# Performance work log

Measured on AMD Instinct MI355X. Metric: run time of the kernel, lower is better.

## Reference

```python
import jax, jax.numpy as jnp
import numpy as np

EPS = 1e-05


def project_to_poincare_ball(v, eps=EPS):
    # clip norm to < 1 - eps
    norm = jnp.linalg.norm(v, axis=-1, keepdims=True)
    scale = jnp.minimum((1.0 - eps) / (norm + 1e-10), 1.0)
    return v * scale


def setup_inputs() -> dict:
    key = jax.random.key(0)
    k1, k2 = jax.random.split(key)
    B, S, D, V = 2, 2048, 512, 32000
    # scale by 0.02 so typical norms (~0.45) lie inside the unit ball
    hidden_states = jax.random.normal(k1, (B, S, D), dtype=jnp.float32) * 0.02
    weight = jax.random.normal(k2, (V, D), dtype=jnp.float32) * 0.02
    return {"hidden_states": hidden_states, "weight": weight}


def reference(hidden_states, weight):
    eps = EPS
    B, S, D = hidden_states.shape
    x = hidden_states.reshape(-1, D)                 # (N, D)
    x = project_to_poincare_ball(x, eps)
    y = project_to_poincare_ball(weight, eps)        # (V, D)

    x_norm_sq = jnp.sum(x * x, axis=-1, keepdims=True)   # (N, 1)
    y_norm_sq = jnp.sum(y * y, axis=-1)                  # (V,)

    # torch.cdist(p=2, use_mm_for_euclid_dist): ||x-y|| via mm expansion,
    # clamped at 0 before sqrt. NOTE: original code names this diff_norm_sq
    # but it is the (unsquared) distance -- reproduced faithfully.
    sq = x_norm_sq + y_norm_sq[None, :] - 2.0 * (x @ y.T)   # (N, V)
    dist = jnp.sqrt(jnp.maximum(sq, 0.0))

    denom = (1.0 - x_norm_sq) * (1.0 - y_norm_sq)[None, :]  # (N, V)
    argument = 1.0 + 2.0 * dist / (denom + eps)
    argument = jnp.maximum(argument, 1.0 + eps)
    distances = jnp.arccosh(argument)                       # (N, V)

    logits = -distances
    return logits.reshape(B, S, -1)
```

## Files before the change

kernel.cpp:

```cpp
#include <hip/hip_runtime.h>
#include <hip/hip_bf16.h>

#define D_DIM 512
#define EPS 1e-5f
#define BM 128
#define BN 128
#define BK 32
#define KT 16

typedef __attribute__((ext_vector_type(8))) short bf16x8;
typedef __attribute__((ext_vector_type(4))) float f32x4;

__device__ __forceinline__ unsigned short f2bf(float f) {
  unsigned int u = __float_as_uint(f);
  u += 0x7FFFu + ((u >> 16) & 1u);
  return (unsigned short)(u >> 16);
}

__global__ __launch_bounds__(256) void prep_rows2(
    const float* __restrict__ x, const float* __restrict__ w,
    unsigned short* __restrict__ Xbf, unsigned short* __restrict__ Ybf,
    float* __restrict__ xnsq, float* __restrict__ ynsq, int N, int total)
{
  int row  = blockIdx.x * 4 + (threadIdx.x >> 6);
  int lane = threadIdx.x & 63;
  if (row >= total) return;

  const float* src; unsigned short* dst; float* nsq; int r;
  if (row < N) { src = x; dst = Xbf; nsq = xnsq; r = row; }
  else         { src = w; dst = Ybf; nsq = ynsq; r = row - N; }

  const float4* s = (const float4*)(src + (size_t)r * D_DIM);
  float4 v0 = s[lane];
  float4 v1 = s[lane + 64];
  float ss = v0.x*v0.x + v0.y*v0.y + v0.z*v0.z + v0.w*v0.w
           + v1.x*v1.x + v1.y*v1.y + v1.z*v1.z + v1.w*v1.w;
  #pragma unroll
  for (int off = 32; off; off >>= 1) ss += __shfl_xor(ss, off);

  float norm  = sqrtf(ss);
  float scale = fminf((1.0f - EPS) / (norm + 1e-10f), 1.0f);
  if (lane == 0) nsq[r] = ss * scale * scale;

  ushort4 o0, o1;
  o0.x = f2bf(v0.x * scale); o0.y = f2bf(v0.y * scale);
  o0.z = f2bf(v0.z * scale); o0.w = f2bf(v0.w * scale);
  o1.x = f2bf(v1.x * scale); o1.y = f2bf(v1.y * scale);
  o1.z = f2bf(v1.z * scale); o1.w = f2bf(v1.w * scale);

  ushort4* dp = (ushort4*)(dst + (size_t)r * D_DIM);
  dp[lane]      = o0;
  dp[lane + 64] = o1;
}

__global__ __launch_bounds__(256, 3) void hyp_gemm(
    const unsigned short* __restrict__ Xbf, const unsigned short* __restrict__ Ybf,
    const float* __restrict__ xnsq, const float* __restrict__ ynsq,
    float* __restrict__ out, int N, int V)
{
  __shared__ __attribute__((aligned(16))) unsigned short sAB[3][2 * BM * BK];

  int ntV = V / BN;
  int bid = blockIdx.x;

  int local = bid >> 3;
  int bn = local >> 2;
  int bm = (bid & 7) * 4 + (local & 3);

  int tid  = threadIdx.x;
  int wid  = tid >> 6;
  int lane = tid & 63;
  int wm = wid >> 1, wn = wid & 1;

  size_t a_row0 = (size_t)bm * BM;
  size_t b_row0 = (size_t)bn * BN;

  auto STAGE = [&](int slot, int kt) {
    int k0 = kt * BK;
    #pragma unroll
    for (int i = 0; i < 2; ++i) {
      int c = i * 256 + tid;
      const unsigned short* gA = Xbf + (a_row0 + (size_t)(c >> 2)) * D_DIM + k0 + (c & 3) * 8;
      const unsigned short* gB = Ybf + (b_row0 + (size_t)(c >> 2)) * D_DIM + k0 + (c & 3) * 8;
      char* base = (char*)&sAB[slot][0];
      char* lA = base + (size_t)(i * 256 + wid * 64) * 16;
      char* lB = base + 8192 + (size_t)(i * 256 + wid * 64) * 16;
      __builtin_amdgcn_global_load_lds(
          (const __attribute__((address_space(1))) void*)gA,
          (__attribute__((address_space(3))) void*)lA, 16, 0, 0);
      __builtin_amdgcn_global_load_lds(
          (const __attribute__((address_space(1))) void*)gB,
          (__attribute__((address_space(3))) void*)lB, 16, 0, 0);
    }
  };

  int jr = lane & 15;
  int h  = lane >> 4;
  float xnv[4], dxv[4];
  #pragma unroll
  for (int m = 0; m < 4; ++m) {
    float xn = xnsq[bm * BM + wm * 64 + m * 16 + jr];
    xnv[m] = xn; dxv[m] = 1.0f - xn;
  }
  f32x4 ynv[4], dyv[4];
  #pragma unroll
  for (int n = 0; n < 4; ++n) {
    f32x4 y4 = *(const f32x4*)&ynsq[bn * BN + wn * 64 + n * 16 + h * 4];
    ynv[n] = y4;
    dyv[n] = 1.0f - y4;
  }

  f32x4 acc[4][4] = {};
  int r = lane & 15, ko = (lane >> 4) * 8;

  STAGE(0, 0);
  STAGE(1, 1);

  #pragma unroll
  for (int t = 0; t < KT; ++t) {
    if (t == KT - 1) {
      asm volatile("s_waitcnt vmcnt(0)" ::: "memory");
    } else {
      asm volatile("s_waitcnt vmcnt(4)" ::: "memory");
    }
    __builtin_amdgcn_sched_barrier(0);
    __builtin_amdgcn_s_barrier();
    __builtin_amdgcn_sched_barrier(0);

    const unsigned short* sA = &sAB[t % 3][0];
    const unsigned short* sB = sA + BM * BK;
    bf16x8 a[4], b[4];
    #pragma unroll
    for (int m = 0; m < 4; ++m)
      a[m] = *(const bf16x8*)&sA[(wm * 64 + m * 16 + r) * BK + ko];
    #pragma unroll
    for (int n = 0; n < 4; ++n)
      b[n] = *(const bf16x8*)&sB[(wn * 64 + n * 16 + r) * BK + ko];

    if (t + 2 < KT) STAGE((t + 2) % 3, t + 2);

    #pragma unroll
    for (int m = 0; m < 4; ++m)
      #pragma unroll
      for (int n = 0; n < 4; ++n)
        acc[m][n] = __builtin_amdgcn_mfma_f32_16x16x32_bf16(b[n], a[m], acc[m][n], 0, 0, 0);
  }

  __syncthreads();
  float* epi = (float*)&sAB[0][0] + wid * (16 * 68);

  float cmv[4];
  #pragma unroll
  for (int m = 0; m < 4; ++m) cmv[m] = 2.0f * __builtin_amdgcn_rcpf(dxv[m]);
  f32x4 rdy[4];
  #pragma unroll
  for (int n = 0; n < 4; ++n) {
    #pragma unroll
    for (int q = 0; q < 4; ++q) rdy[n][q] = __builtin_amdgcn_rcpf(dyv[n][q]);
  }

  size_t out_row0 = (size_t)bm * BM + wm * 64;
  int    out_col0 = bn * BN + wn * 64;

  #pragma unroll
  for (int m = 0; m < 4; ++m) {
    float xn = xnv[m], cm = cmv[m];
    #pragma unroll
    for (int n = 0; n < 4; ++n) {
      f32x4 f;
      #pragma unroll
      for (int q = 0; q < 4; ++q) {
        float dot  = acc[m][n][q];
        float sq   = fmaxf(xn + ynv[n][q] - 2.0f * dot, 0.0f);
        float dist = __builtin_amdgcn_sqrtf(sq);
        float arg  = fmaf(dist * cm, rdy[n][q], 1.0f);
        arg = fmaxf(arg, 1.0f + EPS);
        float t2 = __builtin_amdgcn_sqrtf(fmaf(arg, arg, -1.0f));
        f[q] = -__logf(arg + t2);
      }
      *(f32x4*)&epi[jr * 68 + n * 16 + h * 4] = f;
    }
    #pragma unroll
    for (int k = 0; k < 4; ++k) {
      int xl = k * 4 + h;
      f32x4 f = *(const f32x4*)&epi[xl * 68 + jr * 4];
      size_t rg = out_row0 + m * 16 + xl;
      int    cg = out_col0 + jr * 4;
      __builtin_nontemporal_store(f, (f32x4*)(out + rg * (size_t)V + cg));
    }
  }
}

extern "C" void kernel_launch(void* const* d_in, const int* in_sizes, int n_in,
                              void* d_out, int out_size, void* d_ws, size_t ws_size,
                              hipStream_t stream) {
  const float* x = (const float*)d_in[0];
  const float* w = (const float*)d_in[1];
  float* out = (float*)d_out;

  int N = in_sizes[0] / D_DIM;
  int V = in_sizes[1] / D_DIM;

  char* ws = (char*)d_ws;
  unsigned short* Xbf = (unsigned short*)ws;
  size_t xbf_bytes = (size_t)N * D_DIM * 2;
  unsigned short* Ybf = (unsigned short*)(ws + xbf_bytes);
  size_t ybf_bytes = (size_t)V * D_DIM * 2;
  float* xnsq = (float*)(ws + xbf_bytes + ybf_bytes);
  float* ynsq = xnsq + N;

  int total = N + V;
  prep_rows2<<<dim3((total + 3) / 4), dim3(256), 0, stream>>>(
      x, w, Xbf, Ybf, xnsq, ynsq, N, total);

  int nwg = (N / BM) * (V / BN);
  hyp_gemm<<<dim3(nwg), dim3(256), 0, stream>>>(Xbf, Ybf, xnsq, ynsq, out, N, V);
}
```

Before: 230.0 us.

## Give each wave private LDS tiles, drop block barriers, swizzle LDS slots

Each wave now stages its own 64-row A and B slices into a private double-buffered LDS region, so the per-iteration block-wide s_barrier and the pre-epilogue __syncthreads are removed. An XOR swizzle on the 16-byte k-slot is applied on the global_load_lds side and matched on the fragment reads to reduce LDS bank conflicts. The block-ID mapping drops the grouped raster for a simple row-major tile order, and occupancy is lowered to 2 blocks per CU because LDS use grows. The trade-off is that A and B tiles shared across waves are now loaded twice from global/L2, and the simpler raster may hurt L2 reuse.

Result: slower. 265.7 us (+15.5%).

```diff
diff --git a/kernel.cpp b/kernel.cpp
--- a/kernel.cpp
+++ b/kernel.cpp
@@ -53,44 +53,47 @@
   dp[lane + 64] = o1;
 }
 
-__global__ __launch_bounds__(256, 3) void hyp_gemm(
+__global__ __launch_bounds__(256, 2) void hyp_gemm(
     const unsigned short* __restrict__ Xbf, const unsigned short* __restrict__ Ybf,
     const float* __restrict__ xnsq, const float* __restrict__ ynsq,
     float* __restrict__ out, int N, int V)
 {
-  __shared__ __attribute__((aligned(16))) unsigned short sAB[3][2 * BM * BK];
-
-  int ntV = V / BN;
+  __shared__ __attribute__((aligned(16))) unsigned short lds[4][2][4096];
+
   int bid = blockIdx.x;
-
-  int local = bid >> 3;
-  int bn = local >> 2;
-  int bm = (bid & 7) * 4 + (local & 3);
+  int bm = bid & 31;
+  int bn = bid >> 5;
 
   int tid  = threadIdx.x;
   int wid  = tid >> 6;
   int lane = tid & 63;
   int wm = wid >> 1, wn = wid & 1;
 
-  size_t a_row0 = (size_t)bm * BM;
-  size_t b_row0 = (size_t)bn * BN;
-
-  auto STAGE = [&](int slot, int kt) {
+  size_t a_row0 = (size_t)bm * BM + wm * 64;
+  size_t b_row0 = (size_t)bn * BN + wn * 64;
+
+  auto STAGE = [&](int buf, int kt) {
     int k0 = kt * BK;
-    #pragma unroll
-    for (int i = 0; i < 2; ++i) {
-      int c = i * 256 + tid;
-      const unsigned short* gA = Xbf + (a_row0 + (size_t)(c >> 2)) * D_DIM + k0 + (c & 3) * 8;
-      const unsigned short* gB = Ybf + (b_row0 + (size_t)(c >> 2)) * D_DIM + k0 + (c & 3) * 8;
-      char* base = (char*)&sAB[slot][0];
-      char* lA = base + (size_t)(i * 256 + wid * 64) * 16;
-      char* lB = base + 8192 + (size_t)(i * 256 + wid * 64) * 16;
+    char* base = (char*)&lds[wid][buf][0];
+    #pragma unroll
+    for (int j = 0; j < 4; ++j) {
+      int c = j * 64 + lane;
+      int row = c >> 2;
+      int s = (c & 3) ^ ((row >> 1) & 3);
+      const unsigned short* g = Xbf + (a_row0 + row) * D_DIM + k0 + s * 8;
       __builtin_amdgcn_global_load_lds(
-          (const __attribute__((address_space(1))) void*)gA,
-          (__attribute__((address_space(3))) void*)lA, 16, 0, 0);
+          (const __attribute__((address_space(1))) void*)g,
+          (__attribute__((address_space(3))) void*)(base + j * 1024), 16, 0, 0);
+    }
+    #pragma unroll
+    for (int j = 0; j < 4; ++j) {
+      int c = j * 64 + lane;
+      int row = c >> 2;
+      int s = (c & 3) ^ ((row >> 1) & 3);
+      const unsigned short* g = Ybf + (b_row0 + row) * D_DIM + k0 + s * 8;
       __builtin_amdgcn_global_load_lds(
-          (const __attribute__((address_space(1))) void*)gB,
-          (__attribute__((address_space(3))) void*)lB, 16, 0, 0);
+          (const __attribute__((address_space(1))) void*)g,
+          (__attribute__((address_space(3))) void*)(base + 4096 + j * 1024), 16, 0, 0);
     }
   };
 
@@ -111,7 +114,8 @@
   }
 
   f32x4 acc[4][4] = {};
-  int r = lane & 15, ko = (lane >> 4) * 8;
+  int r = lane & 15;
+  int slotoff = ((lane >> 4) ^ ((r >> 1) & 3)) * 8;
 
   STAGE(0, 0);
   STAGE(1, 1);
@@ -121,23 +125,23 @@
     if (t == KT - 1) {
       asm volatile("s_waitcnt vmcnt(0)" ::: "memory");
     } else {
-      asm volatile("s_waitcnt vmcnt(4)" ::: "memory");
+      asm volatile("s_waitcnt vmcnt(8)" ::: "memory");
     }
     __builtin_amdgcn_sched_barrier(0);
-    __builtin_amdgcn_s_barrier();
+
+    const unsigned short* sbuf = &lds[wid][t & 1][0];
+    bf16x8 a[4], b[4];
+    #pragma unroll
+    for (int m = 0; m < 4; ++m)
+      a[m] = *(const bf16x8*)&sbuf[(m * 16 + r) * 32 + slotoff];
+    #pragma unroll
+    for (int n = 0; n < 4; ++n)
+      b[n] = *(const bf16x8*)&sbuf[2048 + (n * 16 + r) * 32 + slotoff];
+
+    asm volatile("s_waitcnt lgkmcnt(0)" ::: "memory");
     __builtin_amdgcn_sched_barrier(0);
 
-    const unsigned short* sA = &sAB[t % 3][0];
-    const unsigned short* sB = sA + BM * BK;
-    bf16x8 a[4], b[4];
-    #pragma unroll
-    for (int m = 0; m < 4; ++m)
-      a[m] = *(const bf16x8*)&sA[(wm * 64 + m * 16 + r) * BK + ko];
-    #pragma unroll
-    for (int n = 0; n < 4; ++n)
-      b[n] = *(const bf16x8*)&sB[(wn * 64 + n * 16 + r) * BK + ko];
-
-    if (t + 2 < KT) STAGE((t + 2) % 3, t + 2);
+    if (t + 2 < KT) STAGE(t & 1, t + 2);
 
     #pragma unroll
     for (int m = 0; m < 4; ++m)
@@ -146,8 +150,7 @@
         acc[m][n] = __builtin_amdgcn_mfma_f32_16x16x32_bf16(b[n], a[m], acc[m][n], 0, 0, 0);
   }
 
-  __syncthreads();
-  float* epi = (float*)&sAB[0][0] + wid * (16 * 68);
+  float* epi = (float*)&lds[wid][0][0];
 
   float cmv[4];
   #pragma unroll
```
